# Optimization experiments

Measured on AMD Instinct MI355X. Metric: run time of the kernel, lower is better.

The kernel has to match this reference:

```python
import jax, jax.numpy as jnp
import numpy as np

B, T, M, P = 1024, 128, 256, 256  # batch, timesteps, encoder_hidden, decoder_hidden
Tm1 = T - 1


def setup_inputs() -> dict:
    key = jax.random.key(0)
    ks = jax.random.split(key, 10)
    s = lambda k, shape: jax.random.normal(k, shape, jnp.float32) * 0.05
    return {
        "X_encoded": jax.random.normal(ks[0], (B, Tm1, M), jnp.float32),
        "y_prev": jax.random.normal(ks[1], (B, Tm1), jnp.float32),
        # attn_layer: Linear(2P+M -> M), Tanh, Linear(M -> 1)
        "attn_W1": s(ks[2], (M, 2 * P + M)),
        "attn_b1": jnp.zeros((M,), jnp.float32),
        "attn_W2": s(ks[3], (1, M)),
        "attn_b2": jnp.zeros((1,), jnp.float32),
        # LSTM(input_size=1, hidden=P), gate order i,f,g,o
        "W_ih": s(ks[4], (4 * P, 1)),
        "W_hh": s(ks[5], (4 * P, P)),
        "b_ih": jnp.zeros((4 * P,), jnp.float32),
        "b_hh": jnp.zeros((4 * P,), jnp.float32),
        # fc: Linear(M+1 -> 1) (weights init'd normal_() in torch)
        "fc_W": jax.random.normal(ks[6], (1, M + 1), jnp.float32),
        "fc_b": jnp.zeros((1,), jnp.float32),
        # fc_final: Linear(P+M -> 1)
        "fcf_W": s(ks[7], (1, P + M)),
        "fcf_b": jnp.zeros((1,), jnp.float32),
    }


def reference(X_encoded, y_prev, attn_W1, attn_b1, attn_W2, attn_b2,
              W_ih, W_hh, b_ih, b_hh, fc_W, fc_b, fcf_W, fcf_b):
    Bsz, Tsteps, Mdim = X_encoded.shape
    Pdim = W_hh.shape[1]

    def step(carry, y_t):
        d, c, _ = carry  # d,c: [B,P]
        dm = jnp.broadcast_to(d[:, None, :], (Bsz, Tsteps, Pdim))
        cm = jnp.broadcast_to(c[:, None, :], (Bsz, Tsteps, Pdim))
        x = jnp.concatenate([dm, cm, X_encoded], axis=2)  # [B,T-1,2P+M]
        e = jnp.tanh(jnp.einsum('bti,hi->bth', x, attn_W1) + attn_b1)
        scores = jnp.einsum('bth,oh->bto', e, attn_W2)[..., 0] + attn_b2[0]  # [B,T-1]
        beta = jax.nn.softmax(scores, axis=-1)
        context = jnp.einsum('bt,btm->bm', beta, X_encoded)  # [B,M]
        y_tilde = jnp.concatenate([context, y_t[:, None]], axis=1) @ fc_W.T + fc_b  # [B,1]
        gates = y_tilde @ W_ih.T + d @ W_hh.T + (b_ih + b_hh)  # [B,4P]
        i, f, g, o = jnp.split(gates, 4, axis=1)
        c_new = jax.nn.sigmoid(f) * c + jax.nn.sigmoid(i) * jnp.tanh(g)
        d_new = jax.nn.sigmoid(o) * jnp.tanh(c_new)
        return (d_new, c_new, context), None

    init = (jnp.zeros((Bsz, Pdim), X_encoded.dtype),
            jnp.zeros((Bsz, Pdim), X_encoded.dtype),
            jnp.zeros((Bsz, Mdim), X_encoded.dtype))
    (d, c, context), _ = jax.lax.scan(step, init, y_prev.T)  # scan over T-1 steps
    y_pred = jnp.concatenate([d, context], axis=1) @ fcf_W.T + fcf_b  # [B,1]
    return y_pred
```

## Files before the change

kernel.cpp:

```cpp
#include <hip/hip_runtime.h>
#include <hip/hip_bf16.h>

#define TT 127
#define L2E 1.4426950408889634f

typedef __attribute__((ext_vector_type(8))) short s8v;
typedef __attribute__((ext_vector_type(4))) float f4v;
typedef __attribute__((ext_vector_type(4))) int i4v;

__device__ __forceinline__ float bf2f(unsigned short u){
  union { unsigned int i; float f; } v; v.i = ((unsigned int)u) << 16; return v.f;
}
__device__ __forceinline__ unsigned short f2bf(float f){
  union { float f; unsigned int i; } v; v.f = f;
  unsigned int r = v.i + 0x7FFFu + ((v.i >> 16) & 1u);
  return (unsigned short)(r >> 16);
}
__device__ __forceinline__ float fexp2(float x){ return __builtin_amdgcn_exp2f(x); }
__device__ __forceinline__ float frcp(float x){ return __builtin_amdgcn_rcpf(x); }
__device__ __forceinline__ float sigm(float x){
  return frcp(1.f + fexp2(-L2E * x));
}
__device__ __forceinline__ float tanh_f(float x){
  return 1.f - 2.f * frcp(1.f + fexp2(2.f * L2E * x));
}
__device__ __forceinline__ f4v mfma16(s8v a, s8v b, f4v c){
  return __builtin_amdgcn_mfma_f32_16x16x32_bf16(a, b, c, 0, 0, 0);
}
__device__ __forceinline__ void barrier_lgkm(){
  asm volatile("s_waitcnt lgkmcnt(0)" ::: "memory");
  __builtin_amdgcn_s_barrier();
}

__global__ void k_pack_w1dc(const float* __restrict__ W1, unsigned short* __restrict__ WP){
  int n = blockIdx.x * 256 + threadIdx.x;
  int lane = n & 63, w = (n >> 6) & 15, kt = n >> 10;
  int h = w * 16 + (lane & 15);
  int i0 = kt * 32 + (lane >> 4) * 8;
  #pragma unroll
  for (int j = 0; j < 8; ++j)
    WP[(size_t)n * 8 + j] = f2bf(W1[h * 768 + i0 + j]);
}
__global__ void k_pack_whh(const float* __restrict__ Whh, unsigned short* __restrict__ WP){
  int n = blockIdx.x * 256 + threadIdx.x;
  int lane = n & 63, w = (n >> 6) & 15, f = n >> 10;
  int ct = f >> 3, kt = f & 7;
  int g = (w * 4 + ct) * 16 + (lane & 15);
  int i0 = kt * 32 + (lane >> 4) * 8;
  #pragma unroll
  for (int j = 0; j < 8; ++j)
    WP[131072 + (size_t)n * 8 + j] = f2bf(Whh[g * 256 + i0 + j]);
}

__global__ void k_tr_w1x(const float* __restrict__ W1, float* __restrict__ W1xT){
  int idx = blockIdx.x * 256 + threadIdx.x;
  int k = idx >> 8, h = idx & 255;
  W1xT[idx] = W1[h * 768 + 512 + k];
}

__global__ void k_xfg(const float* __restrict__ X, const float* __restrict__ fcW,
                      const float* __restrict__ fcfW,
                      float* __restrict__ xf, float* __restrict__ xg){
  const int b = blockIdx.x;
  const int w = threadIdx.x >> 6, lane = threadIdx.x & 63;
  f4v wf = *(const f4v*)&fcW[lane * 4];
  f4v wg = *(const f4v*)&fcfW[256 + lane * 4];
  for (int t = w; t < TT; t += 4) {
    f4v x = *(const f4v*)&X[((size_t)b * TT + t) * 256 + lane * 4];
    float af = x[0]*wf[0] + x[1]*wf[1] + x[2]*wf[2] + x[3]*wf[3];
    float ag = x[0]*wg[0] + x[1]*wg[1] + x[2]*wg[2] + x[3]*wg[3];
    #pragma unroll
    for (int m = 32; m; m >>= 1) { af += __shfl_xor(af, m); ag += __shfl_xor(ag, m); }
    if (lane == 0) { xf[(size_t)b * TT + t] = af; xg[(size_t)b * TT + t] = ag; }
  }
}

__global__ __launch_bounds__(256) void k_gemm_tx(
    const float* __restrict__ X, const float* __restrict__ W1xT,
    const float* __restrict__ b1, char* __restrict__ Tx8)
{
  __shared__ float As[16][64];
  __shared__ float Bs[16][64];
  const int row0 = blockIdx.x * 64;
  const int col0 = blockIdx.y * 64;
  const int tid = threadIdx.x;
  const int tx = tid & 15, ty = tid >> 4;
  float acc[4][4] = {};
  for (int k0 = 0; k0 < 256; k0 += 16) {
    {
      const int rr = tid & 63, kk4 = (tid >> 6) << 2;
      float4 v = *(const float4*)&X[(size_t)(row0 + rr) * 256 + k0 + kk4];
      As[kk4 + 0][rr] = v.x; As[kk4 + 1][rr] = v.y;
      As[kk4 + 2][rr] = v.z; As[kk4 + 3][rr] = v.w;
    }
    {
      const int cc = tid & 63, kb = tid >> 6;
      #pragma unroll
      for (int j = 0; j < 4; ++j)
        Bs[kb + 4 * j][cc] = W1xT[(size_t)(k0 + kb + 4 * j) * 256 + col0 + cc];
    }
    __syncthreads();
    #pragma unroll
    for (int kk = 0; kk < 16; ++kk) {
      float4 a4 = *(const float4*)&As[kk][ty << 2];
      float4 b4 = *(const float4*)&Bs[kk][tx << 2];
      float av[4] = {a4.x, a4.y, a4.z, a4.w};
      float bv[4] = {b4.x, b4.y, b4.z, b4.w};
      #pragma unroll
      for (int i = 0; i < 4; ++i)
        #pragma unroll
        for (int j = 0; j < 4; ++j)
          acc[i][j] = fmaf(av[i], bv[j], acc[i][j]);
    }
    __syncthreads();
  }
  const int c = col0 + (tx << 2);
  #pragma unroll
  for (int i = 0; i < 4; ++i) {
    const int r = row0 + (ty << 2) + i;
    uchar4 o;
    o.x = (unsigned char)(char)rintf(tanhf(acc[i][0] + b1[c + 0]) * 127.f);
    o.y = (unsigned char)(char)rintf(tanhf(acc[i][1] + b1[c + 1]) * 127.f);
    o.z = (unsigned char)(char)rintf(tanhf(acc[i][2] + b1[c + 2]) * 127.f);
    o.w = (unsigned char)(char)rintf(tanhf(acc[i][3] + b1[c + 3]) * 127.f);
    *(uchar4*)&Tx8[(size_t)r * 256 + c] = o;
  }
}

__global__ __launch_bounds__(1024, 4) void k_main(
    const char* __restrict__ Tx8,
    const unsigned short* __restrict__ WP,
    const float* __restrict__ xf,
    const float* __restrict__ xg,
    const float* __restrict__ yprev,
    const float* __restrict__ W2,
    const float* __restrict__ Wih,
    const float* __restrict__ bih,
    const float* __restrict__ bhh,
    const float* __restrict__ fcW,
    const float* __restrict__ fcb,
    const float* __restrict__ fcfW,
    const float* __restrict__ fcfb,
    float* __restrict__ out)
{
  __shared__ __align__(16) char wring[6 * 16384];
  __shared__ __align__(16) char dcA8[16 * 1152];
  __shared__ __align__(16) float us_s[4][320];
  __shared__ __align__(16) float sc[4][128];
  __shared__ __align__(16) float gts[4][1024];
  __shared__ float w2s[256];
  __shared__ float fcfw_s[256];
  __shared__ float wih_s[1024];
  __shared__ float bsum_s[1024];
  __shared__ float yp_s[4][128];
  __shared__ float xf_s[4][128];
  __shared__ float xg_s[4][128];
  __shared__ float ytil[4];
  __shared__ float sg_s[4];

  const int tid = threadIdx.x;
  const int lane = tid & 63;
  const int w = tid >> 6;
  const int bb = tid >> 8;
  const int hq = tid & 255;
  const int b0 = blockIdx.x << 2;
  const int bq = w >> 2;
  const int cc = lane & 15;
  const int g4 = lane >> 4;

  if (tid < 256) w2s[tid] = W2[tid];
  if (tid >= 256 && tid < 512) fcfw_s[tid - 256] = fcfW[tid - 256];
  wih_s[tid] = Wih[tid];
  bsum_s[tid] = bih[tid] + bhh[tid];
  if (tid < 512 && (tid & 127) < TT)
    yp_s[tid >> 7][tid & 127] = yprev[(size_t)(b0 + (tid >> 7)) * TT + (tid & 127)];
  if (tid >= 512) {
    const int r = (tid - 512) >> 7, c = tid & 127;
    float vf = 0.f, vg = 0.f;
    if (c < TT) {
      vf = xf[(size_t)(b0 + r) * TT + c];
      vg = xg[(size_t)(b0 + r) * TT + c];
    }
    xf_s[r][c] = vf;
    xg_s[r][c] = vg;
  }
  for (int i = tid; i < 16 * 1152 / 2; i += 1024)
    ((unsigned short*)dcA8)[i] = 0;
  const float fcw256 = fcW[256];
  const float fcb0 = fcb[0];
  const float fcfb0 = fcfb[0];
  float creg = 0.f, dreg = 0.f;
  barrier_lgkm();

  const int arow = lane & 15;
  const char* arbase = dcA8 + arow * 1152;
  const int sx4 = (arow & 7) << 4;
  const int g16 = (lane >> 4) << 4;
  const int wlo = w * 1024 + lane * 16;
  const char* WPc = (const char*)WP;
  const char* wslice = wring + wlo;
  char* wdst = wring + w * 1024;

  #pragma unroll
  for (int F = 0; F < 6; ++F) {
    __builtin_amdgcn_global_load_lds((const unsigned int*)(WPc + (size_t)F * 16384 + wlo),
                                     (unsigned int*)(wdst + F * 16384), 16, 0, 0);
  }
  asm volatile("s_waitcnt vmcnt(5)" ::: "memory");
  __builtin_amdgcn_sched_barrier(0);
  s8v bnext = *(const s8v*)(wslice);

  for (int t = 0; t < TT; ++t) {
    {
      f4v au0 = {0.f,0.f,0.f,0.f}, au1 = au0;
      f4v ag0 = au0, ag1 = au0, ag2 = au0, ag3 = au0;
      #pragma unroll
      for (int f = 0; f < 48; ++f) {
        s8v bcur = bnext;
        asm volatile("s_waitcnt vmcnt(4)" ::: "memory");
        __builtin_amdgcn_sched_barrier(0);
        bnext = *(const s8v*)(wslice + (((f + 1) % 6) * 16384));
        const int kt = (f < 16) ? f : (f & 7);
        s8v av = *(const s8v*)(arbase + ((kt * 64 + g16) ^ sx4));
        if (f < 16) {
          if (f & 1) au1 = mfma16(av, bcur, au1);
          else       au0 = mfma16(av, bcur, au0);
        } else if (f < 24) {
          ag0 = mfma16(av, bcur, ag0);
        } else if (f < 32) {
          ag1 = mfma16(av, bcur, ag1);
        } else if (f < 40) {
          ag2 = mfma16(av, bcur, ag2);
        } else {
          ag3 = mfma16(av, bcur, ag3);
        }
        const int nf = (f + 6) % 48;
        __builtin_amdgcn_global_load_lds((const unsigned int*)(WPc + (size_t)nf * 16384 + wlo),
                                         (unsigned int*)(wdst + (f % 6) * 16384), 16, 0, 0);
      }
      f4v au = au0 + au1;
      #pragma unroll
      for (int r = 0; r < 4; ++r) {
        au[r] += __shfl_xor(au[r], 16);
        ag0[r] += __shfl_xor(ag0[r], 16);
        ag1[r] += __shfl_xor(ag1[r], 16);
        ag2[r] += __shfl_xor(ag2[r], 16);
        ag3[r] += __shfl_xor(ag3[r], 16);
      }
      if (lane < 16) {
        const int hp = w * 20 + lane;
        #pragma unroll
        for (int r = 0; r < 4; ++r)
          us_s[r][hp] = tanh_f(au[r]);
        #pragma unroll
        for (int r = 0; r < 4; ++r) {
          gts[r][(w * 4 + 0) * 16 + lane] = ag0[r];
          gts[r][(w * 4 + 1) * 16 + lane] = ag1[r];
          gts[r][(w * 4 + 2) * 16 + lane] = ag2[r];
          gts[r][(w * 4 + 3) * 16 + lane] = ag3[r];
        }
      }
    }
    barrier_lgkm();

    {
      float tur[16], w2r[16], wt127[16];
      #pragma unroll
      for (int e4 = 0; e4 < 4; ++e4) {
        f4v tv = *(const f4v*)&us_s[bq][cc * 20 + e4 * 4];
        f4v wv = *(const f4v*)&w2s[cc * 16 + e4 * 4];
        #pragma unroll
        for (int j = 0; j < 4; ++j) {
          tur[e4*4+j] = tv[j];
          w2r[e4*4+j] = wv[j];
          wt127[e4*4+j] = wv[j] * tv[j] * 127.f;
        }
      }
      const char* txb = &Tx8[((size_t)(b0 + bq) * TT) * 256 + cc * 16];
      #pragma unroll
      for (int it = 0; it < 8; ++it) {
        const int tt = it * 16 + (w & 3) * 4 + g4;
        const int ttc = tt < 126 ? tt : 126;
        i4v dv = __builtin_nontemporal_load((const i4v*)(txb + (size_t)ttc * 256));
        float acc = 0.f;
        #pragma unroll
        for (int j = 0; j < 4; ++j) {
          const int d = dv[j];
          const float x0 = (float)((d << 24) >> 24);
          const float x1 = (float)((d << 16) >> 24);
          const float x2 = (float)((d << 8) >> 24);
          const float x3 = (float)(d >> 24);
          const int e = j * 4;
          acc = fmaf(fmaf(w2r[e+0], x0, wt127[e+0]), frcp(fmaf(tur[e+0], x0, 127.f)), acc);
          acc = fmaf(fmaf(w2r[e+1], x1, wt127[e+1]), frcp(fmaf(tur[e+1], x1, 127.f)), acc);
          acc = fmaf(fmaf(w2r[e+2], x2, wt127[e+2]), frcp(fmaf(tur[e+2], x2, 127.f)), acc);
          acc = fmaf(fmaf(w2r[e+3], x3, wt127[e+3]), frcp(fmaf(tur[e+3], x3, 127.f)), acc);
        }
        acc += __shfl_xor(acc, 1);
        acc += __shfl_xor(acc, 2);
        acc += __shfl_xor(acc, 4);
        acc += __shfl_xor(acc, 8);
        if (cc == 0 && tt < TT) sc[bq][tt] = acc;
      }
    }
    barrier_lgkm();

    if (w < 4) {
      const float s0 = sc[w][lane];
      const float s1 = (lane < 63) ? sc[w][lane + 64] : -3.0e38f;
      float mx = fmaxf(s0, s1);
      #pragma unroll
      for (int m = 32; m; m >>= 1) mx = fmaxf(mx, __shfl_xor(mx, m));
      const float p0 = fexp2((s0 - mx) * L2E);
      const float p1 = (lane < 63) ? fexp2((s1 - mx) * L2E) : 0.f;
      float sm = p0 + p1;
      float af = fmaf(p0, xf_s[w][lane], p1 * xf_s[w][(lane + 64) & 127]);
      #pragma unroll
      for (int m = 32; m; m >>= 1) {
        sm += __shfl_xor(sm, m);
        af += __shfl_xor(af, m);
      }
      const float inv = frcp(sm);
      if (lane == 0)
        ytil[w] = af * inv + fcw256 * yp_s[w][t] + fcb0;
      if (t == TT - 1) {
        float ag_ = fmaf(p0, xg_s[w][lane], p1 * xg_s[w][(lane + 64) & 127]);
        #pragma unroll
        for (int m = 32; m; m >>= 1) ag_ += __shfl_xor(ag_, m);
        if (lane == 0) sg_s[w] = ag_ * inv;
      }
    }
    barrier_lgkm();

    {
      const float yt = ytil[bb];
      const float gi = gts[bb][hq]       + yt * wih_s[hq]       + bsum_s[hq];
      const float gf = gts[bb][hq + 256] + yt * wih_s[hq + 256] + bsum_s[hq + 256];
      const float gg = gts[bb][hq + 512] + yt * wih_s[hq + 512] + bsum_s[hq + 512];
      const float go = gts[bb][hq + 768] + yt * wih_s[hq + 768] + bsum_s[hq + 768];
      creg = sigm(gf) * creg + sigm(gi) * tanh_f(gg);
      dreg = sigm(go) * tanh_f(creg);
      const unsigned short dh = f2bf(dreg);
      const unsigned short dl = f2bf(dreg - bf2f(dh));
      const unsigned short ch = f2bf(creg);
      const unsigned short cl = f2bf(creg - bf2f(ch));
      const int cd = 2 * hq;
      const int ccol = 512 + 2 * hq;
      const int sh = (bb & 7) << 4;
      const int sl = ((bb + 4) & 7) << 4;
      *(unsigned short*)(dcA8 + bb * 1152       + (((cd & ~15) ^ sh) | (cd & 15)))   = dh;
      *(unsigned short*)(dcA8 + (bb + 4) * 1152 + (((cd & ~15) ^ sl) | (cd & 15)))   = dl;
      *(unsigned short*)(dcA8 + bb * 1152       + (((ccol & ~15) ^ sh) | (ccol & 15))) = ch;
      *(unsigned short*)(dcA8 + (bb + 4) * 1152 + (((ccol & ~15) ^ sl) | (ccol & 15))) = cl;
    }
    barrier_lgkm();
  }

  us_s[bb][hq] = dreg;
  barrier_lgkm();
  if (w < 4) {
    float a = 0.f;
    #pragma unroll
    for (int j = 0; j < 4; ++j) {
      const int m = lane + (j << 6);
      a = fmaf(us_s[w][m], fcfw_s[m], a);
    }
    #pragma unroll
    for (int m = 32; m; m >>= 1) a += __shfl_xor(a, m);
    if (lane == 0) out[b0 + w] = a + sg_s[w] + fcfb0;
  }
  asm volatile("s_waitcnt vmcnt(0)" ::: "memory");
}

extern "C" void kernel_launch(void* const* d_in, const int* in_sizes, int n_in,
                              void* d_out, int out_size, void* d_ws, size_t ws_size,
                              hipStream_t stream) {
  const float* X    = (const float*)d_in[0];
  const float* yprev= (const float*)d_in[1];
  const float* W1   = (const float*)d_in[2];
  const float* b1   = (const float*)d_in[3];
  const float* W2   = (const float*)d_in[4];
  const float* Wih  = (const float*)d_in[6];
  const float* Whh  = (const float*)d_in[7];
  const float* bih  = (const float*)d_in[8];
  const float* bhh  = (const float*)d_in[9];
  const float* fcW  = (const float*)d_in[10];
  const float* fcb  = (const float*)d_in[11];
  const float* fcfW = (const float*)d_in[12];
  const float* fcfb = (const float*)d_in[13];
  float* out = (float*)d_out;

  size_t off = 0;
  char* base = (char*)d_ws;
  auto alloc = [&](size_t bytes) -> void* {
    void* p = base + off;
    off += (bytes + 255) & ~(size_t)255;
    return p;
  };
  char* Tx8            = (char*)alloc((size_t)1024 * TT * 256);
  unsigned short* WP   = (unsigned short*)alloc((size_t)48 * 16384);
  float* W1xT          = (float*)alloc((size_t)256 * 256 * 4);
  float* xf            = (float*)alloc((size_t)1024 * TT * 4);
  float* xg            = (float*)alloc((size_t)1024 * TT * 4);
  (void)in_sizes; (void)n_in; (void)out_size; (void)ws_size;

  k_pack_w1dc<<<64, 256, 0, stream>>>(W1, WP);
  k_pack_whh<<<128, 256, 0, stream>>>(Whh, WP);
  k_tr_w1x<<<256, 256, 0, stream>>>(W1, W1xT);
  k_xfg<<<1024, 256, 0, stream>>>(X, fcW, fcfW, xf, xg);
  dim3 gg(2032, 4);
  k_gemm_tx<<<gg, 256, 0, stream>>>(X, W1xT, b1, Tx8);
  k_main<<<256, 1024, 0, stream>>>(Tx8, WP, xf, xg, yprev, W2,
                                   Wih, bih, bhh, fcW, fcb, fcfW, fcfb, out);
}
```

Before: 4.427 ms.

## Transpose Tx layout per hidden chunk and fuse score, softmax and LSTM phases

The precomputed int8 tanh(X·W1x) tensor is now stored grouped by 16-column chunk and then timestep, so each wave reads only its own hidden slice for all timesteps. Wave-local partial scores go to a shared parts buffer, and every wave reduces them itself, which removes the cross-lane shuffle reduction and two block barriers per step. The weight ring shrinks from 6 to 4 stages and the prefetch is issued before the MFMA, freeing LDS at the cost of a shallower prefetch depth. Softmax, y_tilde and the gate update are merged into one phase, with softmax work repeated redundantly across waves.

```diff
diff --git a/kernel.cpp b/kernel.cpp
--- a/kernel.cpp
+++ b/kernel.cpp
@@ -77,7 +77,7 @@
 
 __global__ __launch_bounds__(256) void k_gemm_tx(
     const float* __restrict__ X, const float* __restrict__ W1xT,
-    const float* __restrict__ b1, char* __restrict__ Tx8)
+    const float* __restrict__ b1, char* __restrict__ TxT)
 {
   __shared__ float As[16][64];
   __shared__ float Bs[16][64];
@@ -118,17 +118,18 @@
   #pragma unroll
   for (int i = 0; i < 4; ++i) {
     const int r = row0 + (ty << 2) + i;
+    const int b = r / TT, t = r % TT;
     uchar4 o;
     o.x = (unsigned char)(char)rintf(tanhf(acc[i][0] + b1[c + 0]) * 127.f);
     o.y = (unsigned char)(char)rintf(tanhf(acc[i][1] + b1[c + 1]) * 127.f);
     o.z = (unsigned char)(char)rintf(tanhf(acc[i][2] + b1[c + 2]) * 127.f);
     o.w = (unsigned char)(char)rintf(tanhf(acc[i][3] + b1[c + 3]) * 127.f);
-    *(uchar4*)&Tx8[(size_t)r * 256 + c] = o;
+    *(uchar4*)&TxT[(((size_t)(b * 16 + (c >> 4))) * 128 + t) * 16 + (c & 15)] = o;
   }
 }
 
 __global__ __launch_bounds__(1024, 4) void k_main(
-    const char* __restrict__ Tx8,
+    const char* __restrict__ TxT,
     const unsigned short* __restrict__ WP,
     const float* __restrict__ xf,
     const float* __restrict__ xg,
@@ -143,10 +144,10 @@
     const float* __restrict__ fcfb,
     float* __restrict__ out)
 {
-  __shared__ __align__(16) char wring[6 * 16384];
+  __shared__ __align__(16) char wring[4 * 16384];
   __shared__ __align__(16) char dcA8[16 * 1152];
-  __shared__ __align__(16) float us_s[4][320];
-  __shared__ __align__(16) float sc[4][128];
+  __shared__ __align__(16) float us_w[16][4][16];
+  __shared__ __align__(16) float parts[16][4][129];
   __shared__ __align__(16) float gts[4][1024];
   __shared__ float w2s[256];
   __shared__ float fcfw_s[256];
@@ -155,25 +156,23 @@
   __shared__ float yp_s[4][128];
   __shared__ float xf_s[4][128];
   __shared__ float xg_s[4][128];
-  __shared__ float ytil[4];
   __shared__ float sg_s[4];
 
   const int tid = threadIdx.x;
   const int lane = tid & 63;
   const int w = tid >> 6;
-  const int bb = tid >> 8;
-  const int hq = tid & 255;
+  const int hq = (w & 3) * 64 + lane;
   const int b0 = blockIdx.x << 2;
   const int bq = w >> 2;
-  const int cc = lane & 15;
-  const int g4 = lane >> 4;
 
   if (tid < 256) w2s[tid] = W2[tid];
   if (tid >= 256 && tid < 512) fcfw_s[tid - 256] = fcfW[tid - 256];
   wih_s[tid] = Wih[tid];
   bsum_s[tid] = bih[tid] + bhh[tid];
-  if (tid < 512 && (tid & 127) < TT)
-    yp_s[tid >> 7][tid & 127] = yprev[(size_t)(b0 + (tid >> 7)) * TT + (tid & 127)];
+  if (tid < 512) {
+    const int r = tid >> 7, c = tid & 127;
+    yp_s[r][c] = (c < TT) ? yprev[(size_t)(b0 + r) * TT + c] : 0.f;
+  }
   if (tid >= 512) {
     const int r = (tid - 512) >> 7, c = tid & 127;
     float vf = 0.f, vg = 0.f;
@@ -202,11 +201,11 @@
   char* wdst = wring + w * 1024;
 
   #pragma unroll
-  for (int F = 0; F < 6; ++F) {
+  for (int F = 0; F < 4; ++F) {
     __builtin_amdgcn_global_load_lds((const unsigned int*)(WPc + (size_t)F * 16384 + wlo),
                                      (unsigned int*)(wdst + F * 16384), 16, 0, 0);
   }
-  asm volatile("s_waitcnt vmcnt(5)" ::: "memory");
+  asm volatile("s_waitcnt vmcnt(3)" ::: "memory");
   __builtin_amdgcn_sched_barrier(0);
   s8v bnext = *(const s8v*)(wslice);
 
@@ -217,9 +216,12 @@
       #pragma unroll
       for (int f = 0; f < 48; ++f) {
         s8v bcur = bnext;
-        asm volatile("s_waitcnt vmcnt(4)" ::: "memory");
+        asm volatile("s_waitcnt vmcnt(2)" ::: "memory");
         __builtin_amdgcn_sched_barrier(0);
-        bnext = *(const s8v*)(wslice + (((f + 1) % 6) * 16384));
+        bnext = *(const s8v*)(wslice + (((f + 1) & 3) * 16384));
+        const int nf = (f + 4) % 48;
+        __builtin_amdgcn_global_load_lds((const unsigned int*)(WPc + (size_t)nf * 16384 + wlo),
+                                         (unsigned int*)(wdst + (f & 3) * 16384), 16, 0, 0);
         const int kt = (f < 16) ? f : (f & 7);
         s8v av = *(const s8v*)(arbase + ((kt * 64 + g16) ^ sx4));
         if (f < 16) {
@@ -234,9 +236,6 @@
         } else {
           ag3 = mfma16(av, bcur, ag3);
         }
-        const int nf = (f + 6) % 48;
-        __builtin_amdgcn_global_load_lds((const unsigned int*)(WPc + (size_t)nf * 16384 + wlo),
-                                         (unsigned int*)(wdst + (f % 6) * 16384), 16, 0, 0);
       }
       f4v au = au0 + au1;
       #pragma unroll
@@ -248,10 +247,9 @@
         ag3[r] += __shfl_xor(ag3[r], 16);
       }
       if (lane < 16) {
-        const int hp = w * 20 + lane;
         #pragma unroll
         for (int r = 0; r < 4; ++r)
-          us_s[r][hp] = tanh_f(au[r]);
+          us_w[w][r][lane] = tanh_f(au[r]);
         #pragma unroll
         for (int r = 0; r < 4; ++r) {
           gts[r][(w * 4 + 0) * 16 + lane] = ag0[r];
@@ -260,84 +258,78 @@
           gts[r][(w * 4 + 3) * 16 + lane] = ag3[r];
         }
       }
+      asm volatile("s_waitcnt lgkmcnt(0)" ::: "memory");
+      __builtin_amdgcn_sched_barrier(0);
+    }
+
+    {
+      #pragma unroll
+      for (int b2 = 0; b2 < 4; ++b2) {
+        float tur[16], w2r[16], wt127[16];
+        #pragma unroll
+        for (int e = 0; e < 16; ++e) {
+          tur[e] = us_w[w][b2][e];
+          w2r[e] = w2s[w * 16 + e];
+          wt127[e] = w2r[e] * tur[e] * 127.f;
+        }
+        const char* txb = TxT + ((size_t)(b0 + b2) * 16 + w) * 2048;
+        #pragma unroll
+        for (int rep = 0; rep < 2; ++rep) {
+          const int tt = rep * 64 + lane;
+          const int ttc = tt < 126 ? tt : 126;
+          i4v dv = *(const i4v*)(txb + (size_t)ttc * 16);
+          float acc = 0.f;
+          #pragma unroll
+          for (int j = 0; j < 4; ++j) {
+            const int d = dv[j];
+            const float x0 = (float)((d << 24) >> 24);
+            const float x1 = (float)((d << 16) >> 24);
+            const float x2 = (float)((d << 8) >> 24);
+            const float x3 = (float)(d >> 24);
+            const int e = j * 4;
+            acc = fmaf(fmaf(w2r[e+0], x0, wt127[e+0]), frcp(fmaf(tur[e+0], x0, 127.f)), acc);
+            acc = fmaf(fmaf(w2r[e+1], x1, wt127[e+1]), frcp(fmaf(tur[e+1], x1, 127.f)), acc);
+            acc = fmaf(fmaf(w2r[e+2], x2, wt127[e+2]), frcp(fmaf(tur[e+2], x2, 127.f)), acc);
+            acc = fmaf(fmaf(w2r[e+3], x3, wt127[e+3]), frcp(fmaf(tur[e+3], x3, 127.f)), acc);
+          }
+          parts[w][b2][tt] = acc;
+        }
+      }
     }
     barrier_lgkm();
 
     {
-      float tur[16], w2r[16], wt127[16];
-      #pragma unroll
-      for (int e4 = 0; e4 < 4; ++e4) {
-        f4v tv = *(const f4v*)&us_s[bq][cc * 20 + e4 * 4];
-        f4v wv = *(const f4v*)&w2s[cc * 16 + e4 * 4];
-        #pragma unroll
-        for (int j = 0; j < 4; ++j) {
-          tur[e4*4+j] = tv[j];
-          w2r[e4*4+j] = wv[j];
-          wt127[e4*4+j] = wv[j] * tv[j] * 127.f;
-        }
-      }
-      const char* txb = &Tx8[((size_t)(b0 + bq) * TT) * 256 + cc * 16];
-      #pragma unroll
-      for (int it = 0; it < 8; ++it) {
-        const int tt = it * 16 + (w & 3) * 4 + g4;
-        const int ttc = tt < 126 ? tt : 126;
-        i4v dv = __builtin_nontemporal_load((const i4v*)(txb + (size_t)ttc * 256));
-        float acc = 0.f;
-        #pragma unroll
-        for (int j = 0; j < 4; ++j) {
-          const int d = dv[j];
-          const float x0 = (float)((d << 24) >> 24);
-          const float x1 = (float)((d << 16) >> 24);
-          const float x2 = (float)((d << 8) >> 24);
-          const float x3 = (float)(d >> 24);
-          const int e = j * 4;
-          acc = fmaf(fmaf(w2r[e+0], x0, wt127[e+0]), frcp(fmaf(tur[e+0], x0, 127.f)), acc);
-          acc = fmaf(fmaf(w2r[e+1], x1, wt127[e+1]), frcp(fmaf(tur[e+1], x1, 127.f)), acc);
-          acc = fmaf(fmaf(w2r[e+2], x2, wt127[e+2]), frcp(fmaf(tur[e+2], x2, 127.f)), acc);
-          acc = fmaf(fmaf(w2r[e+3], x3, wt127[e+3]), frcp(fmaf(tur[e+3], x3, 127.f)), acc);
-        }
-        acc += __shfl_xor(acc, 1);
-        acc += __shfl_xor(acc, 2);
-        acc += __shfl_xor(acc, 4);
-        acc += __shfl_xor(acc, 8);
-        if (cc == 0 && tt < TT) sc[bq][tt] = acc;
-      }
-    }
-    barrier_lgkm();
-
-    if (w < 4) {
-      const float s0 = sc[w][lane];
-      const float s1 = (lane < 63) ? sc[w][lane + 64] : -3.0e38f;
-      float mx = fmaxf(s0, s1);
+      float s0 = 0.f, s1 = 0.f;
+      #pragma unroll
+      for (int ww = 0; ww < 16; ++ww) {
+        s0 += parts[ww][bq][lane];
+        s1 += parts[ww][bq][lane + 64];
+      }
+      const float s1m = (lane < 63) ? s1 : -3.0e38f;
+      float mx = fmaxf(s0, s1m);
       #pragma unroll
       for (int m = 32; m; m >>= 1) mx = fmaxf(mx, __shfl_xor(mx, m));
       const float p0 = fexp2((s0 - mx) * L2E);
-      const float p1 = (lane < 63) ? fexp2((s1 - mx) * L2E) : 0.f;
+      const float p1 = (lane < 63) ? fexp2((s1m - mx) * L2E) : 0.f;
       float sm = p0 + p1;
-      float af = fmaf(p0, xf_s[w][lane], p1 * xf_s[w][(lane + 64) & 127]);
+      float af = fmaf(p0, xf_s[bq][lane], p1 * xf_s[bq][(lane + 64) & 127]);
       #pragma unroll
       for (int m = 32; m; m >>= 1) {
         sm += __shfl_xor(sm, m);
         af += __shfl_xor(af, m);
       }
       const float inv = frcp(sm);
-      if (lane == 0)
-        ytil[w] = af * inv + fcw256 * yp_s[w][t] + fcb0;
+      const float yt = af * inv + fcw256 * yp_s[bq][t] + fcb0;
       if (t == TT - 1) {
-        float ag_ = fmaf(p0, xg_s[w][lane], p1 * xg_s[w][(lane + 64) & 127]);
+        float ag_ = fmaf(p0, xg_s[bq][lane], p1 * xg_s[bq][(lane + 64) & 127]);
         #pragma unroll
         for (int m = 32; m; m >>= 1) ag_ += __shfl_xor(ag_, m);
-        if (lane == 0) sg_s[w] = ag_ * inv;
-      }
-    }
-    barrier_lgkm();
-
-    {
-      const float yt = ytil[bb];
-      const float gi = gts[bb][hq]       + yt * wih_s[hq]       + bsum_s[hq];
-      const float gf = gts[bb][hq + 256] + yt * wih_s[hq + 256] + bsum_s[hq + 256];
-      const float gg = gts[bb][hq + 512] + yt * wih_s[hq + 512] + bsum_s[hq + 512];
-      const float go = gts[bb][hq + 768] + yt * wih_s[hq + 768] + bsum_s[hq + 768];
+        if ((w & 3) == 0 && lane == 0) sg_s[bq] = ag_ * inv;
+      }
+      const float gi = gts[bq][hq]       + yt * wih_s[hq]       + bsum_s[hq];
+      const float gf = gts[bq][hq + 256] + yt * wih_s[hq + 256] + bsum_s[hq + 256];
+      const float gg = gts[bq][hq + 512] + yt * wih_s[hq + 512] + bsum_s[hq + 512];
+      const float go = gts[bq][hq + 768] + yt * wih_s[hq + 768] + bsum_s[hq + 768];
       creg = sigm(gf) * creg + sigm(gi) * tanh_f(gg);
       dreg = sigm(go) * tanh_f(creg);
       const unsigned short dh = f2bf(dreg);
@@ -346,24 +338,24 @@
       const unsigned short cl = f2bf(creg - bf2f(ch));
       const int cd = 2 * hq;
       const int ccol = 512 + 2 * hq;
-      const int sh = (bb & 7) << 4;
-      const int sl = ((bb + 4) & 7) << 4;
-      *(unsigned short*)(dcA8 + bb * 1152       + (((cd & ~15) ^ sh) | (cd & 15)))   = dh;
-      *(unsigned short*)(dcA8 + (bb + 4) * 1152 + (((cd & ~15) ^ sl) | (cd & 15)))   = dl;
-      *(unsigned short*)(dcA8 + bb * 1152       + (((ccol & ~15) ^ sh) | (ccol & 15))) = ch;
-      *(unsigned short*)(dcA8 + (bb + 4) * 1152 + (((ccol & ~15) ^ sl) | (ccol & 15))) = cl;
+      const int sh = (bq & 7) << 4;
+      const int sl = ((bq + 4) & 7) << 4;
+      *(unsigned short*)(dcA8 + bq * 1152       + (((cd & ~15) ^ sh) | (cd & 15)))   = dh;
+      *(unsigned short*)(dcA8 + (bq + 4) * 1152 + (((cd & ~15) ^ sl) | (cd & 15)))   = dl;
+      *(unsigned short*)(dcA8 + bq * 1152       + (((ccol & ~15) ^ sh) | (ccol & 15))) = ch;
+      *(unsigned short*)(dcA8 + (bq + 4) * 1152 + (((ccol & ~15) ^ sl) | (ccol & 15))) = cl;
     }
     barrier_lgkm();
   }
 
-  us_s[bb][hq] = dreg;
+  ((float*)parts)[bq * 256 + hq] = dreg;
   barrier_lgkm();
   if (w < 4) {
     float a = 0.f;
     #pragma unroll
     for (int j = 0; j < 4; ++j) {
       const int m = lane + (j << 6);
-      a = fmaf(us_s[w][m], fcfw_s[m], a);
+      a = fmaf(((const float*)parts)[w * 256 + m], fcfw_s[m], a);
     }
     #pragma unroll
     for (int m = 32; m; m >>= 1) a += __shfl_xor(a, m);
@@ -397,7 +389,7 @@
     off += (bytes + 255) & ~(size_t)255;
     return p;
   };
-  char* Tx8            = (char*)alloc((size_t)1024 * TT * 256);
+  char* TxT            = (char*)alloc((size_t)1024 * 16 * 128 * 16);
   unsigned short* WP   = (unsigned short*)alloc((size_t)48 * 16384);
   float* W1xT          = (float*)alloc((size_t)256 * 256 * 4);
   float* xf            = (float*)alloc((size_t)1024 * TT * 4);
@@ -409,7 +401,7 @@
   k_tr_w1x<<<256, 256, 0, stream>>>(W1, W1xT);
   k_xfg<<<1024, 256, 0, stream>>>(X, fcW, fcfW, xf, xg);
   dim3 gg(2032, 4);
-  k_gemm_tx<<<gg, 256, 0, stream>>>(X, W1xT, b1, Tx8);
-  k_main<<<256, 1024, 0, stream>>>(Tx8, WP, xf, xg, yprev, W2,
+  k_gemm_tx<<<gg, 256, 0, stream>>>(X, W1xT, b1, TxT);
+  k_main<<<256, 1024, 0, stream>>>(TxT, WP, xf, xg, yprev, W2,
                                    Wih, bih, bhh, fcW, fcb, fcfW, fcfb, out);
 }
```

Measured after the change: 4.574 ms. 3.3% more time.

## Keep per-batch int8 attention tile resident in LDS, stream weights from global

Applied to the files above, without the earlier changes.

The precomputed int8 tanh(X·W1x) tile for the block's 4 batch rows is repacked into a swizzled layout by the GEMM kernel and loaded once into a 128KB LDS buffer. Each step then reads it from LDS instead of re-streaming it from global memory. To free LDS, the weight ring buffer is dropped and the recurrent weights are read directly from global (L2) with a 3-register prefetch. Several small shared tables (W2, Wih, biases, xf/xg, yprev) now come straight from global memory, and the dc operand buffer is shrunk to 9 rows. The trade is more global and L2 traffic for the weights and small scalars on every step, in exchange for no per-step HBM reads of the large int8 tensor.

```diff
diff --git a/kernel.cpp b/kernel.cpp
--- a/kernel.cpp
+++ b/kernel.cpp
@@ -77,7 +77,7 @@
 
 __global__ __launch_bounds__(256) void k_gemm_tx(
     const float* __restrict__ X, const float* __restrict__ W1xT,
-    const float* __restrict__ b1, char* __restrict__ Tx8)
+    const float* __restrict__ b1, char* __restrict__ TxP)
 {
   __shared__ float As[16][64];
   __shared__ float Bs[16][64];
@@ -115,20 +115,22 @@
     __syncthreads();
   }
   const int c = col0 + (tx << 2);
+  const int ccf = c >> 4, ef = c & 15;
   #pragma unroll
   for (int i = 0; i < 4; ++i) {
     const int r = row0 + (ty << 2) + i;
+    const int b = r / TT, t = r % TT;
     uchar4 o;
     o.x = (unsigned char)(char)rintf(tanhf(acc[i][0] + b1[c + 0]) * 127.f);
     o.y = (unsigned char)(char)rintf(tanhf(acc[i][1] + b1[c + 1]) * 127.f);
     o.z = (unsigned char)(char)rintf(tanhf(acc[i][2] + b1[c + 2]) * 127.f);
     o.w = (unsigned char)(char)rintf(tanhf(acc[i][3] + b1[c + 3]) * 127.f);
-    *(uchar4*)&Tx8[(size_t)r * 256 + c] = o;
+    *(uchar4*)&TxP[(size_t)b * 32768 + ccf * 2048 + (((t << 4) ^ ((ccf & 7) << 4))) + ef] = o;
   }
 }
 
 __global__ __launch_bounds__(1024, 4) void k_main(
-    const char* __restrict__ Tx8,
+    const char* __restrict__ TxP,
     const unsigned short* __restrict__ WP,
     const float* __restrict__ xf,
     const float* __restrict__ xg,
@@ -143,18 +145,11 @@
     const float* __restrict__ fcfb,
     float* __restrict__ out)
 {
-  __shared__ __align__(16) char wring[6 * 16384];
-  __shared__ __align__(16) char dcA8[16 * 1152];
-  __shared__ __align__(16) float us_s[4][320];
+  __shared__ __align__(16) char TxL[131072];
+  __shared__ __align__(16) char dcA8[9 * 1040];
+  __shared__ __align__(16) float us4[1024];
   __shared__ __align__(16) float sc[4][128];
   __shared__ __align__(16) float gts[4][1024];
-  __shared__ float w2s[256];
-  __shared__ float fcfw_s[256];
-  __shared__ float wih_s[1024];
-  __shared__ float bsum_s[1024];
-  __shared__ float yp_s[4][128];
-  __shared__ float xf_s[4][128];
-  __shared__ float xg_s[4][128];
   __shared__ float ytil[4];
   __shared__ float sg_s[4];
 
@@ -168,76 +163,59 @@
   const int cc = lane & 15;
   const int g4 = lane >> 4;
 
-  if (tid < 256) w2s[tid] = W2[tid];
-  if (tid >= 256 && tid < 512) fcfw_s[tid - 256] = fcfW[tid - 256];
-  wih_s[tid] = Wih[tid];
-  bsum_s[tid] = bih[tid] + bhh[tid];
-  if (tid < 512 && (tid & 127) < TT)
-    yp_s[tid >> 7][tid & 127] = yprev[(size_t)(b0 + (tid >> 7)) * TT + (tid & 127)];
-  if (tid >= 512) {
-    const int r = (tid - 512) >> 7, c = tid & 127;
-    float vf = 0.f, vg = 0.f;
-    if (c < TT) {
-      vf = xf[(size_t)(b0 + r) * TT + c];
-      vg = xg[(size_t)(b0 + r) * TT + c];
-    }
-    xf_s[r][c] = vf;
-    xg_s[r][c] = vg;
-  }
-  for (int i = tid; i < 16 * 1152 / 2; i += 1024)
+  for (int i = tid; i < 9 * 1040 / 2; i += 1024)
     ((unsigned short*)dcA8)[i] = 0;
   const float fcw256 = fcW[256];
   const float fcb0 = fcb[0];
   const float fcfb0 = fcfb[0];
   float creg = 0.f, dreg = 0.f;
-  barrier_lgkm();
+
+  const int wlo = w * 1024 + lane * 16;
+  {
+    const char* src = TxP + (size_t)b0 * 32768;
+    #pragma unroll
+    for (int i = 0; i < 8; ++i)
+      __builtin_amdgcn_global_load_lds((const unsigned int*)(src + (size_t)i * 16384 + wlo),
+                                       (unsigned int*)(TxL + i * 16384 + w * 1024), 16, 0, 0);
+  }
+  const char* wb = (const char*)WP + wlo;
+  s8v wv0 = *(const s8v*)(wb);
+  s8v wv1 = *(const s8v*)(wb + 16384);
+  s8v wv2 = *(const s8v*)(wb + 2 * 16384);
 
   const int arow = lane & 15;
-  const char* arbase = dcA8 + arow * 1152;
+  const int rowi = arow < 8 ? arow : 8;
+  const char* arbase = dcA8 + rowi * 1040;
   const int sx4 = (arow & 7) << 4;
-  const int g16 = (lane >> 4) << 4;
-  const int wlo = w * 1024 + lane * 16;
-  const char* WPc = (const char*)WP;
-  const char* wslice = wring + wlo;
-  char* wdst = wring + w * 1024;
-
-  #pragma unroll
-  for (int F = 0; F < 6; ++F) {
-    __builtin_amdgcn_global_load_lds((const unsigned int*)(WPc + (size_t)F * 16384 + wlo),
-                                     (unsigned int*)(wdst + F * 16384), 16, 0, 0);
-  }
-  asm volatile("s_waitcnt vmcnt(5)" ::: "memory");
-  __builtin_amdgcn_sched_barrier(0);
-  s8v bnext = *(const s8v*)(wslice);
+  const int g16 = g4 << 4;
+  const char* txl = TxL + bq * 32768 + cc * 2048;
+  const int ccx = (cc & 7) << 4;
+
+  asm volatile("s_waitcnt vmcnt(0) lgkmcnt(0)" ::: "memory");
+  __builtin_amdgcn_s_barrier();
 
   for (int t = 0; t < TT; ++t) {
     {
       f4v au0 = {0.f,0.f,0.f,0.f}, au1 = au0;
       f4v ag0 = au0, ag1 = au0, ag2 = au0, ag3 = au0;
-      #pragma unroll
-      for (int f = 0; f < 48; ++f) {
-        s8v bcur = bnext;
-        asm volatile("s_waitcnt vmcnt(4)" ::: "memory");
-        __builtin_amdgcn_sched_barrier(0);
-        bnext = *(const s8v*)(wslice + (((f + 1) % 6) * 16384));
-        const int kt = (f < 16) ? f : (f & 7);
-        s8v av = *(const s8v*)(arbase + ((kt * 64 + g16) ^ sx4));
-        if (f < 16) {
-          if (f & 1) au1 = mfma16(av, bcur, au1);
-          else       au0 = mfma16(av, bcur, au0);
-        } else if (f < 24) {
-          ag0 = mfma16(av, bcur, ag0);
-        } else if (f < 32) {
-          ag1 = mfma16(av, bcur, ag1);
-        } else if (f < 40) {
-          ag2 = mfma16(av, bcur, ag2);
-        } else {
-          ag3 = mfma16(av, bcur, ag3);
-        }
-        const int nf = (f + 6) % 48;
-        __builtin_amdgcn_global_load_lds((const unsigned int*)(WPc + (size_t)nf * 16384 + wlo),
-                                         (unsigned int*)(wdst + (f % 6) * 16384), 16, 0, 0);
-      }
+      #define PROC(F, BC) { \
+        const int kt_ = ((F) < 16) ? (F) : ((F) & 7); \
+        s8v av_ = *(const s8v*)(arbase + ((kt_ * 64 + g16) ^ sx4)); \
+        if ((F) < 16) { if ((F) & 1) au1 = mfma16(av_, BC, au1); else au0 = mfma16(av_, BC, au0); } \
+        else if ((F) < 24) ag0 = mfma16(av_, BC, ag0); \
+        else if ((F) < 32) ag1 = mfma16(av_, BC, ag1); \
+        else if ((F) < 40) ag2 = mfma16(av_, BC, ag2); \
+        else               ag3 = mfma16(av_, BC, ag3); }
+      #pragma unroll
+      for (int f3 = 0; f3 < 48; f3 += 3) {
+        PROC(f3 + 0, wv0)
+        wv0 = *(const s8v*)(wb + (size_t)((f3 + 3) % 48) * 16384);
+        PROC(f3 + 1, wv1)
+        wv1 = *(const s8v*)(wb + (size_t)((f3 + 4) % 48) * 16384);
+        PROC(f3 + 2, wv2)
+        wv2 = *(const s8v*)(wb + (size_t)((f3 + 5) % 48) * 16384);
+      }
+      #undef PROC
       f4v au = au0 + au1;
       #pragma unroll
       for (int r = 0; r < 4; ++r) {
@@ -248,10 +226,9 @@
         ag3[r] += __shfl_xor(ag3[r], 16);
       }
       if (lane < 16) {
-        const int hp = w * 20 + lane;
         #pragma unroll
         for (int r = 0; r < 4; ++r)
-          us_s[r][hp] = tanh_f(au[r]);
+          us4[r * 256 + w * 16 + ((((lane >> 2) ^ (w & 3)) << 2) | (lane & 3))] = tanh_f(au[r]);
         #pragma unroll
         for (int r = 0; r < 4; ++r) {
           gts[r][(w * 4 + 0) * 16 + lane] = ag0[r];
@@ -267,8 +244,8 @@
       float tur[16], w2r[16], wt127[16];
       #pragma unroll
       for (int e4 = 0; e4 < 4; ++e4) {
-        f4v tv = *(const f4v*)&us_s[bq][cc * 20 + e4 * 4];
-        f4v wv = *(const f4v*)&w2s[cc * 16 + e4 * 4];
+        f4v tv = *(const f4v*)&us4[bq * 256 + cc * 16 + ((e4 ^ (cc & 3)) << 2)];
+        f4v wv = *(const f4v*)&W2[cc * 16 + e4 * 4];
         #pragma unroll
         for (int j = 0; j < 4; ++j) {
           tur[e4*4+j] = tv[j];
@@ -276,12 +253,11 @@
           wt127[e4*4+j] = wv[j] * tv[j] * 127.f;
         }
       }
-      const char* txb = &Tx8[((size_t)(b0 + bq) * TT) * 256 + cc * 16];
       #pragma unroll
       for (int it = 0; it < 8; ++it) {
         const int tt = it * 16 + (w & 3) * 4 + g4;
         const int ttc = tt < 126 ? tt : 126;
-        i4v dv = __builtin_nontemporal_load((const i4v*)(txb + (size_t)ttc * 256));
+        i4v dv = *(const i4v*)(txl + (((ttc << 4) ^ ccx)));
         float acc = 0.f;
         #pragma unroll
         for (int j = 0; j < 4; ++j) {
@@ -313,8 +289,10 @@
       for (int m = 32; m; m >>= 1) mx = fmaxf(mx, __shfl_xor(mx, m));
       const float p0 = fexp2((s0 - mx) * L2E);
       const float p1 = (lane < 63) ? fexp2((s1 - mx) * L2E) : 0.f;
+      const float xfv0 = xf[(size_t)(b0 + w) * TT + lane];
+      const float xfv1 = (lane < 63) ? xf[(size_t)(b0 + w) * TT + lane + 64] : 0.f;
       float sm = p0 + p1;
-      float af = fmaf(p0, xf_s[w][lane], p1 * xf_s[w][(lane + 64) & 127]);
+      float af = fmaf(p0, xfv0, p1 * xfv1);
       #pragma unroll
       for (int m = 32; m; m >>= 1) {
         sm += __shfl_xor(sm, m);
@@ -322,9 +300,11 @@
       }
       const float inv = frcp(sm);
       if (lane == 0)
-        ytil[w] = af * inv + fcw256 * yp_s[w][t] + fcb0;
+        ytil[w] = af * inv + fcw256 * yprev[(size_t)(b0 + w) * TT + t] + fcb0;
       if (t == TT - 1) {
-        float ag_ = fmaf(p0, xg_s[w][lane], p1 * xg_s[w][(lane + 64) & 127]);
+        const float xgv0 = xg[(size_t)(b0 + w) * TT + lane];
+        const float xgv1 = (lane < 63) ? xg[(size_t)(b0 + w) * TT + lane + 64] : 0.f;
+        float ag_ = fmaf(p0, xgv0, p1 * xgv1);
         #pragma unroll
         for (int m = 32; m; m >>= 1) ag_ += __shfl_xor(ag_, m);
         if (lane == 0) sg_s[w] = ag_ * inv;
@@ -334,10 +314,10 @@
 
     {
       const float yt = ytil[bb];
-      const float gi = gts[bb][hq]       + yt * wih_s[hq]       + bsum_s[hq];
-      const float gf = gts[bb][hq + 256] + yt * wih_s[hq + 256] + bsum_s[hq + 256];
-      const float gg = gts[bb][hq + 512] + yt * wih_s[hq + 512] + bsum_s[hq + 512];
-      const float go = gts[bb][hq + 768] + yt * wih_s[hq + 768] + bsum_s[hq + 768];
+      const float gi = gts[bb][hq]       + yt * Wih[hq]       + bih[hq]       + bhh[hq];
+      const float gf = gts[bb][hq + 256] + yt * Wih[hq + 256] + bih[hq + 256] + bhh[hq + 256];
+      const float gg = gts[bb][hq + 512] + yt * Wih[hq + 512] + bih[hq + 512] + bhh[hq + 512];
+      const float go = gts[bb][hq + 768] + yt * Wih[hq + 768] + bih[hq + 768] + bhh[hq + 768];
       creg = sigm(gf) * creg + sigm(gi) * tanh_f(gg);
       dreg = sigm(go) * tanh_f(creg);
       const unsigned short dh = f2bf(dreg);
@@ -348,22 +328,22 @@
       const int ccol = 512 + 2 * hq;
       const int sh = (bb & 7) << 4;
       const int sl = ((bb + 4) & 7) << 4;
-      *(unsigned short*)(dcA8 + bb * 1152       + (((cd & ~15) ^ sh) | (cd & 15)))   = dh;
-      *(unsigned short*)(dcA8 + (bb + 4) * 1152 + (((cd & ~15) ^ sl) | (cd & 15)))   = dl;
-      *(unsigned short*)(dcA8 + bb * 1152       + (((ccol & ~15) ^ sh) | (ccol & 15))) = ch;
-      *(unsigned short*)(dcA8 + (bb + 4) * 1152 + (((ccol & ~15) ^ sl) | (ccol & 15))) = cl;
+      *(unsigned short*)(dcA8 + bb * 1040       + (((cd & ~15) ^ sh) | (cd & 15)))     = dh;
+      *(unsigned short*)(dcA8 + (bb + 4) * 1040 + (((cd & ~15) ^ sl) | (cd & 15)))     = dl;
+      *(unsigned short*)(dcA8 + bb * 1040       + (((ccol & ~15) ^ sh) | (ccol & 15))) = ch;
+      *(unsigned short*)(dcA8 + (bb + 4) * 1040 + (((ccol & ~15) ^ sl) | (ccol & 15))) = cl;
     }
     barrier_lgkm();
   }
 
-  us_s[bb][hq] = dreg;
+  ((float*)gts)[bb * 256 + hq] = dreg;
   barrier_lgkm();
   if (w < 4) {
     float a = 0.f;
     #pragma unroll
     for (int j = 0; j < 4; ++j) {
       const int m = lane + (j << 6);
-      a = fmaf(us_s[w][m], fcfw_s[m], a);
+      a = fmaf(((const float*)gts)[w * 256 + m], fcfW[m], a);
     }
     #pragma unroll
     for (int m = 32; m; m >>= 1) a += __shfl_xor(a, m);
@@ -397,7 +377,7 @@
     off += (bytes + 255) & ~(size_t)255;
     return p;
   };
-  char* Tx8            = (char*)alloc((size_t)1024 * TT * 256);
+  char* TxP            = (char*)alloc((size_t)1024 * 32768);
   unsigned short* WP   = (unsigned short*)alloc((size_t)48 * 16384);
   float* W1xT          = (float*)alloc((size_t)256 * 256 * 4);
   float* xf            = (float*)alloc((size_t)1024 * TT * 4);
@@ -409,7 +389,7 @@
   k_tr_w1x<<<256, 256, 0, stream>>>(W1, W1xT);
   k_xfg<<<1024, 256, 0, stream>>>(X, fcW, fcfW, xf, xg);
   dim3 gg(2032, 4);
-  k_gemm_tx<<<gg, 256, 0, stream>>>(X, W1xT, b1, Tx8);
-  k_main<<<256, 1024, 0, stream>>>(Tx8, WP, xf, xg, yprev, W2,
+  k_gemm_tx<<<gg, 256, 0, stream>>>(X, W1xT, b1, TxP);
+  k_main<<<256, 1024, 0, stream>>>(TxP, WP, xf, xg, yprev, W2,
                                    Wih, bih, bhh, fcW, fcb, fcfW, fcfb, out);
 }
```

Measured after the change: 5.172 ms. 1.17x slower.
